# Performance work log

Measured on AMD Instinct MI355X. Metric: run time of the kernel, lower is better.

The kernel has to match this reference:

```python
import jax, jax.numpy as jnp
import numpy as np

EPS = 1e-6


def setup_inputs() -> dict:
    key = jax.random.key(0)
    kx, ky = jax.random.split(key)
    B, T, N, D = 2, 16, 1024, 3
    x = jax.random.normal(kx, (B, T, N, D), dtype=jnp.float32)
    y = jax.random.normal(ky, (B, T, N, D), dtype=jnp.float32)
    return {"x": x, "y": y}


def reference(x, y):
    B, T, N, _ = x.shape
    xf = x.reshape(B * T, N, -1)  # (BT, N, 3)
    yf = y.reshape(B * T, N, -1)  # (BT, N, 3)
    # Squared pairwise distances via norms + cross term to avoid the
    # (BT, N, N, 3) diff tensor; index i runs over y, j over x, matching
    # dist[b, i, j] = ||x[b, j] - y[b, i]||^2 in the torch code.
    x2 = jnp.sum(xf * xf, axis=-1)               # (BT, N)
    y2 = jnp.sum(yf * yf, axis=-1)               # (BT, N)
    cross = jnp.einsum("bid,bjd->bij", yf, xf)   # (BT, N, N)
    sq = jnp.maximum(y2[:, :, None] + x2[:, None, :] - 2.0 * cross, 0.0)
    dist = jnp.sqrt(EPS + sq)                    # (BT, N, N)
    min1 = jnp.min(dist, axis=1)  # nearest y for each x point -> (BT, N)
    min2 = jnp.min(dist, axis=2)  # nearest x for each y point -> (BT, N)
    return jnp.mean(min1) + jnp.mean(min2)
```

## Files before the change

kernel.cpp:

```cpp
#include <hip/hip_runtime.h>
#include <math.h>

#define EPSF 1e-6f
#define N_PTS 1024
#define BT 32

__global__ __launch_bounds__(256) void chamfer_stage(
    const float* __restrict__ x, const float* __restrict__ y,
    float* __restrict__ ws) {
  const int t   = threadIdx.x;
  const int rc  = blockIdx.x;
  const int b   = blockIdx.y;
  const int dir = blockIdx.z;

  const float* q = dir ? y : x;
  const float* r = dir ? x : y;
  const float* qb = q + (size_t)b * N_PTS * 3;
  const float* rb = r + (size_t)b * N_PTS * 3 + (size_t)rc * 256 * 3;

  __shared__ float4 s[256];
  {
    float rx = rb[t * 3 + 0];
    float ry = rb[t * 3 + 1];
    float rz = rb[t * 3 + 2];
    s[t] = make_float4(rx, ry, rz, 0.0f);
  }
  __syncthreads();

  float qx[4], qy[4], qz[4], m[4];
#pragma unroll
  for (int k = 0; k < 4; ++k) {
    const int j = t + 256 * k;
    qx[k] = qb[j * 3 + 0];
    qy[k] = qb[j * 3 + 1];
    qz[k] = qb[j * 3 + 2];
    m[k] = 3.4e38f;
  }

#pragma unroll 4
  for (int i = 0; i < 256; ++i) {
    const float4 rp = s[i];
#pragma unroll
    for (int k = 0; k < 4; ++k) {
      const float dx = qx[k] - rp.x;
      const float dy = qy[k] - rp.y;
      const float dz = qz[k] - rp.z;
      const float sq = dx * dx + dy * dy + dz * dz;
      m[k] = fminf(m[k], sq);
    }
  }

  float* wbase = ws + (size_t)(dir * BT + b) * (N_PTS * 4);
#pragma unroll
  for (int k = 0; k < 4; ++k) {
    const int j = t + 256 * k;
    wbase[j * 4 + rc] = m[k];
  }
}

__global__ __launch_bounds__(256) void chamfer_reduce(
    const float* __restrict__ ws, float* __restrict__ out) {
  const int g = blockIdx.x * 256 + threadIdx.x;
  const float4 p = ((const float4*)ws)[g];
  const float msq = fminf(fminf(p.x, p.y), fminf(p.z, p.w));
  float d = sqrtf(EPSF + msq);

  for (int off = 32; off > 0; off >>= 1) d += __shfl_down(d, off, 64);

  __shared__ float wsum[4];
  const int lane = threadIdx.x & 63;
  const int w = threadIdx.x >> 6;
  if (lane == 0) wsum[w] = d;
  __syncthreads();
  if (threadIdx.x == 0) {
    const float bsum = wsum[0] + wsum[1] + wsum[2] + wsum[3];
    atomicAdd(out, bsum * (1.0f / 32768.0f));
  }
}

__global__ __launch_bounds__(256) void chamfer_simple(
    const float* __restrict__ x, const float* __restrict__ y,
    float* __restrict__ out) {
  const int t   = threadIdx.x;
  const int qc  = blockIdx.x;
  const int b   = blockIdx.y;
  const int dir = blockIdx.z;

  const float* q = dir ? y : x;
  const float* r = dir ? x : y;
  const float* qb = q + (size_t)b * N_PTS * 3;
  const float* rb = r + (size_t)b * N_PTS * 3;

  __shared__ float4 s[N_PTS];
  for (int i = t; i < N_PTS; i += 256) {
    s[i] = make_float4(rb[i * 3], rb[i * 3 + 1], rb[i * 3 + 2], 0.0f);
  }
  __syncthreads();

  const int j = qc * 256 + t;
  const float qx = qb[j * 3], qy = qb[j * 3 + 1], qz = qb[j * 3 + 2];
  float m = 3.4e38f;
#pragma unroll 8
  for (int i = 0; i < N_PTS; ++i) {
    const float4 rp = s[i];
    const float dx = qx - rp.x;
    const float dy = qy - rp.y;
    const float dz = qz - rp.z;
    m = fminf(m, dx * dx + dy * dy + dz * dz);
  }
  float d = sqrtf(EPSF + m);

  for (int off = 32; off > 0; off >>= 1) d += __shfl_down(d, off, 64);

  __shared__ float wsum[4];
  if ((t & 63) == 0) wsum[t >> 6] = d;
  __syncthreads();
  if (t == 0) {
    atomicAdd(out, (wsum[0] + wsum[1] + wsum[2] + wsum[3]) * (1.0f / 32768.0f));
  }
}

extern "C" void kernel_launch(void* const* d_in, const int* in_sizes, int n_in,
                              void* d_out, int out_size, void* d_ws, size_t ws_size,
                              hipStream_t stream) {
  const float* x = (const float*)d_in[0];
  const float* y = (const float*)d_in[1];
  float* out = (float*)d_out;

  hipMemsetAsync(out, 0, sizeof(float) * out_size, stream);

  const size_t ws_need = (size_t)2 * BT * N_PTS * 4 * sizeof(float);
  if (ws_size >= ws_need) {
    chamfer_stage<<<dim3(4, BT, 2), 256, 0, stream>>>(x, y, (float*)d_ws);
    chamfer_reduce<<<dim3(256), 256, 0, stream>>>((const float*)d_ws, out);
  } else {
    chamfer_simple<<<dim3(4, BT, 2), 256, 0, stream>>>(x, y, out);
  }
}
```

Baseline: 76.30 us.

## Use norm-plus-cross-term distance and split reference points into more blocks

Measured after the change: 71.87 us. 1.06x faster.

```diff
diff --git a/kernel.cpp b/kernel.cpp
--- a/kernel.cpp
+++ b/kernel.cpp
@@ -4,8 +4,10 @@
 #define EPSF 1e-6f
 #define N_PTS 1024
 #define BT 32
+#define RC 16
+#define CHUNK 64
 
-__global__ __launch_bounds__(256) void chamfer_stage(
+__global__ __launch_bounds__(128) void chamfer_stage(
     const float* __restrict__ x, const float* __restrict__ y,
     float* __restrict__ ws) {
   const int t   = threadIdx.x;
@@ -13,68 +15,68 @@
   const int b   = blockIdx.y;
   const int dir = blockIdx.z;
 
-  const float* q = dir ? y : x;
-  const float* r = dir ? x : y;
-  const float* qb = q + (size_t)b * N_PTS * 3;
-  const float* rb = r + (size_t)b * N_PTS * 3 + (size_t)rc * 256 * 3;
+  const float* qarr = dir ? y : x;
+  const float* rarr = dir ? x : y;
+  const float* qb = qarr + (size_t)b * (N_PTS * 3);
+  const float* rb = rarr + (size_t)b * (N_PTS * 3) + (size_t)rc * (CHUNK * 3);
 
-  __shared__ float4 s[256];
-  {
-    float rx = rb[t * 3 + 0];
-    float ry = rb[t * 3 + 1];
-    float rz = rb[t * 3 + 2];
-    s[t] = make_float4(rx, ry, rz, 0.0f);
+  __shared__ float4 s[CHUNK];
+  if (t < CHUNK) {
+    const float rx = rb[t * 3 + 0];
+    const float ry = rb[t * 3 + 1];
+    const float rz = rb[t * 3 + 2];
+    s[t] = make_float4(rx, ry, rz, rx * rx + ry * ry + rz * rz);
   }
   __syncthreads();
 
-  float qx[4], qy[4], qz[4], m[4];
+  float qx[8], qy[8], qz[8], q2[8], m[8];
 #pragma unroll
-  for (int k = 0; k < 4; ++k) {
-    const int j = t + 256 * k;
+  for (int k = 0; k < 8; ++k) {
+    const int j = t + 128 * k;
     qx[k] = qb[j * 3 + 0];
     qy[k] = qb[j * 3 + 1];
     qz[k] = qb[j * 3 + 2];
+    q2[k] = qx[k] * qx[k] + qy[k] * qy[k] + qz[k] * qz[k];
     m[k] = 3.4e38f;
   }
 
 #pragma unroll 4
-  for (int i = 0; i < 256; ++i) {
+  for (int i = 0; i < CHUNK; ++i) {
     const float4 rp = s[i];
 #pragma unroll
-    for (int k = 0; k < 4; ++k) {
-      const float dx = qx[k] - rp.x;
-      const float dy = qy[k] - rp.y;
-      const float dz = qz[k] - rp.z;
-      const float sq = dx * dx + dy * dy + dz * dz;
-      m[k] = fminf(m[k], sq);
+    for (int k = 0; k < 8; ++k) {
+      const float cross = qx[k] * rp.x + qy[k] * rp.y + qz[k] * rp.z;
+      const float v = fmaf(-2.0f, cross, rp.w);
+      m[k] = fminf(m[k], v);
     }
   }
 
-  float* wbase = ws + (size_t)(dir * BT + b) * (N_PTS * 4);
+  float* wbase = ws + ((size_t)(dir * BT + b) * RC + rc) * N_PTS;
 #pragma unroll
-  for (int k = 0; k < 4; ++k) {
-    const int j = t + 256 * k;
-    wbase[j * 4 + rc] = m[k];
+  for (int k = 0; k < 8; ++k) {
+    const int j = t + 128 * k;
+    wbase[j] = fmaxf(q2[k] + m[k], 0.0f);
   }
 }
 
 __global__ __launch_bounds__(256) void chamfer_reduce(
     const float* __restrict__ ws, float* __restrict__ out) {
   const int g = blockIdx.x * 256 + threadIdx.x;
-  const float4 p = ((const float4*)ws)[g];
-  const float msq = fminf(fminf(p.x, p.y), fminf(p.z, p.w));
-  float d = sqrtf(EPSF + msq);
+  const int dirb = g >> 10;
+  const int q = g & (N_PTS - 1);
+  const float* base = ws + (size_t)dirb * RC * N_PTS + q;
+  float mn = base[0];
+#pragma unroll
+  for (int r = 1; r < RC; ++r) mn = fminf(mn, base[r * N_PTS]);
+  float d = sqrtf(EPSF + mn);
 
   for (int off = 32; off > 0; off >>= 1) d += __shfl_down(d, off, 64);
 
   __shared__ float wsum[4];
-  const int lane = threadIdx.x & 63;
-  const int w = threadIdx.x >> 6;
-  if (lane == 0) wsum[w] = d;
+  if ((threadIdx.x & 63) == 0) wsum[threadIdx.x >> 6] = d;
   __syncthreads();
   if (threadIdx.x == 0) {
-    const float bsum = wsum[0] + wsum[1] + wsum[2] + wsum[3];
-    atomicAdd(out, bsum * (1.0f / 32768.0f));
+    atomicAdd(out, (wsum[0] + wsum[1] + wsum[2] + wsum[3]) * (1.0f / 32768.0f));
   }
 }
 
@@ -86,29 +88,29 @@
   const int b   = blockIdx.y;
   const int dir = blockIdx.z;
 
-  const float* q = dir ? y : x;
-  const float* r = dir ? x : y;
-  const float* qb = q + (size_t)b * N_PTS * 3;
-  const float* rb = r + (size_t)b * N_PTS * 3;
+  const float* qarr = dir ? y : x;
+  const float* rarr = dir ? x : y;
+  const float* qb = qarr + (size_t)b * N_PTS * 3;
+  const float* rb = rarr + (size_t)b * N_PTS * 3;
 
   __shared__ float4 s[N_PTS];
   for (int i = t; i < N_PTS; i += 256) {
-    s[i] = make_float4(rb[i * 3], rb[i * 3 + 1], rb[i * 3 + 2], 0.0f);
+    const float rx = rb[i * 3], ry = rb[i * 3 + 1], rz = rb[i * 3 + 2];
+    s[i] = make_float4(rx, ry, rz, rx * rx + ry * ry + rz * rz);
   }
   __syncthreads();
 
   const int j = qc * 256 + t;
   const float qx = qb[j * 3], qy = qb[j * 3 + 1], qz = qb[j * 3 + 2];
+  const float q2 = qx * qx + qy * qy + qz * qz;
   float m = 3.4e38f;
 #pragma unroll 8
   for (int i = 0; i < N_PTS; ++i) {
     const float4 rp = s[i];
-    const float dx = qx - rp.x;
-    const float dy = qy - rp.y;
-    const float dz = qz - rp.z;
-    m = fminf(m, dx * dx + dy * dy + dz * dz);
+    const float cross = qx * rp.x + qy * rp.y + qz * rp.z;
+    m = fminf(m, fmaf(-2.0f, cross, rp.w));
   }
-  float d = sqrtf(EPSF + m);
+  float d = sqrtf(EPSF + fmaxf(q2 + m, 0.0f));
 
   for (int off = 32; off > 0; off >>= 1) d += __shfl_down(d, off, 64);
 
@@ -129,9 +131,9 @@
 
   hipMemsetAsync(out, 0, sizeof(float) * out_size, stream);
 
-  const size_t ws_need = (size_t)2 * BT * N_PTS * 4 * sizeof(float);
+  const size_t ws_need = (size_t)2 * BT * RC * N_PTS * sizeof(float);
   if (ws_size >= ws_need) {
-    chamfer_stage<<<dim3(4, BT, 2), 256, 0, stream>>>(x, y, (float*)d_ws);
+    chamfer_stage<<<dim3(RC, BT, 2), 128, 0, stream>>>(x, y, (float*)d_ws);
     chamfer_reduce<<<dim3(256), 256, 0, stream>>>((const float*)d_ws, out);
   } else {
     chamfer_simple<<<dim3(4, BT, 2), 256, 0, stream>>>(x, y, out);
```
